# Kernel tuning notes

Measured on AMD Instinct MI355X. Metric: run time of the kernel, lower is better.

Reference implementation:

```python
import jax, jax.numpy as jnp
import numpy as np

GRID_DIM = 32      # output crop size
RES = 0.25         # A per voxel
CUBES = 5          # cubes_around_atoms_dim
NUM_CH = 5
BOX = 20.0         # dumb coords pin extents to [-20, 20]^3
LATO = 2 * CUBES + 1                      # 11
D = int(2 * BOX / RES) + 2 * (CUBES + 1) + 1  # 173, static full grid dim


def setup_inputs() -> dict:
    key = jax.random.key(0)
    k1, k2 = jax.random.split(key)
    B, N = 8, 64
    coords = jax.random.uniform(k1, (B, N, 3), jnp.float32, -7.5, 7.5)
    atoms_channel = jax.random.randint(k2, (B, N), 0, NUM_CH).astype(jnp.int32)
    radius = jnp.full((B, N), 0.5, jnp.float32)
    return {"coords": coords, "atoms_channel": atoms_channel, "radius": radius}


def _add_dumb_coords(coords, atoms_channel, radius):
    B = coords.shape[0]
    coords = jnp.concatenate(
        [coords, jnp.full((B, 1, 3), -BOX, coords.dtype), jnp.full((B, 1, 3), BOX, coords.dtype)], axis=1)
    atoms_channel = jnp.concatenate([atoms_channel, jnp.zeros((B, 2), atoms_channel.dtype)], axis=1)
    radius = jnp.concatenate([radius, jnp.full((B, 2), 0.5, radius.dtype)], axis=1)
    return coords, atoms_channel, radius


def reference(coords, atoms_channel, radius):
    coords, atoms_channel, radius = _add_dumb_coords(coords, atoms_channel, radius)
    B, M, _ = coords.shape
    # coordinates in voxel units; translation puts min corner at CUBES+1 cells
    scaled = (coords + BOX) / RES + (CUBES + 1)            # [B,M,3]
    base = jnp.floor(scaled).astype(jnp.int32)             # host voxel of each atom
    r = np.arange(-CUBES, CUBES + 1)
    off = jnp.asarray(np.stack(np.meshgrid(r, r, r, indexing='ij'), -1).reshape(-1, 3), jnp.int32)  # [K,3]
    cell = base[:, :, None, :] + off[None, None]           # [B,M,K,3] grid cells touched
    # squared distance (in A^2) from atom to cell centers; avoids sqrt (smooth at 0)
    delta = scaled[:, :, None, :] - (cell.astype(jnp.float32) + 0.5)
    d2 = jnp.sum(delta * delta, axis=-1) * (RES * RES)     # [B,M,K]
    # gaussian splat: exp(-d^2 / (2 r^2))
    val = jnp.exp(-0.5 * d2 / (radius[:, :, None] ** 2))   # [B,M,K]
    b_idx = jnp.arange(B, dtype=jnp.int32)[:, None, None]
    ch = atoms_channel[:, :, None].astype(jnp.int32)
    flat = (((b_idx * NUM_CH + ch) * D + cell[..., 0]) * D + cell[..., 1]) * D + cell[..., 2]
    vol = jnp.zeros((B * NUM_CH * D * D * D,), jnp.float32)
    vol = vol.at[flat.reshape(-1)].add(val.reshape(-1), mode='drop')
    vol = vol.reshape(B, NUM_CH, D, D, D)
    c = D // 2
    lo, hi = c - GRID_DIM // 2, c + GRID_DIM // 2
    return vol[:, :, lo:hi, lo:hi, lo:hi]
```

## Files before the change

kernel.cpp:

```cpp
#include <hip/hip_runtime.h>

#define B_DIM      8
#define N_ATOMS    64
#define NUM_CH     5
#define GRID_DIM   32
#define CROP_LO    70
#define CROP_HI    101
#define CUBES      5
#define LATO       11
#define KCELLS     (LATO*LATO*LATO)

__global__ __launch_bounds__(256) void zero_out_kernel(float4* __restrict__ out, int n4) {
    int i = blockIdx.x * blockDim.x + threadIdx.x;
    if (i < n4) out[i] = make_float4(0.f, 0.f, 0.f, 0.f);
}

__global__ __launch_bounds__(256) void splat_kernel(
    const float* __restrict__ coords,
    const int*   __restrict__ channel,
    const float* __restrict__ radius,
    float* __restrict__ out)
{
    const int atom = blockIdx.x;
    const int b    = atom >> 6;

    const float sx = coords[3*atom + 0] * 4.0f + 86.0f;
    const float sy = coords[3*atom + 1] * 4.0f + 86.0f;
    const float sz = coords[3*atom + 2] * 4.0f + 86.0f;
    const int bx = (int)floorf(sx);
    const int by = (int)floorf(sy);
    const int bz = (int)floorf(sz);

    if (bx + CUBES < CROP_LO || bx - CUBES > CROP_HI ||
        by + CUBES < CROP_LO || by - CUBES > CROP_HI ||
        bz + CUBES < CROP_LO || bz - CUBES > CROP_HI) return;

    const float r  = radius[atom];
    const float karg = -0.5f * 0.0625f / (r * r);
    const int ch = channel[atom];
    float* outBase = out + ((size_t)(b * NUM_CH + ch)) * (GRID_DIM*GRID_DIM*GRID_DIM);

    for (int k = threadIdx.x; k < KCELLS; k += 256) {
        const int i   = k / (LATO*LATO);
        const int rem = k - i * (LATO*LATO);
        const int j   = rem / LATO;
        const int l   = rem - j * LATO;

        const int gx = bx - CUBES + i;
        const int gy = by - CUBES + j;
        const int gz = bz - CUBES + l;

        const unsigned ux = (unsigned)(gx - CROP_LO);
        const unsigned uy = (unsigned)(gy - CROP_LO);
        const unsigned uz = (unsigned)(gz - CROP_LO);
        if (ux < GRID_DIM && uy < GRID_DIM && uz < GRID_DIM) {
            const float dx = sx - ((float)gx + 0.5f);
            const float dy = sy - ((float)gy + 0.5f);
            const float dz = sz - ((float)gz + 0.5f);
            const float d2 = dx*dx + dy*dy + dz*dz;
            const float val = __expf(d2 * karg);
            atomicAdd(outBase + ((ux * GRID_DIM) + uy) * GRID_DIM + uz, val);
        }
    }
}

extern "C" void kernel_launch(void* const* d_in, const int* in_sizes, int n_in,
                              void* d_out, int out_size, void* d_ws, size_t ws_size,
                              hipStream_t stream) {
    const float* coords  = (const float*)d_in[0];
    const int*   channel = (const int*)d_in[1];
    const float* radius  = (const float*)d_in[2];
    float* out = (float*)d_out;

    const int n4 = out_size / 4;
    hipLaunchKernelGGL(zero_out_kernel, dim3((n4 + 255) / 256), dim3(256), 0, stream,
                       (float4*)out, n4);

    const int atoms = in_sizes[1];
    hipLaunchKernelGGL(splat_kernel, dim3(atoms), dim3(256), 0, stream,
                       coords, channel, radius, out);
}
```

Baseline: 61.09 us.

## Replace atomic scatter splat with per-voxel gather over batch atoms

Swaps the atom-centric scatter (one block per atom doing atomicAdds into a pre-zeroed output) for a voxel-centric gather: each thread owns one output voxel, loops over the 64 atoms of its batch staged in shared memory, and accumulates per-channel sums in registers. This removes the separate zero-fill kernel launch and all global atomics, and writes each output element exactly once. In exchange every voxel tests all 64 atoms, mostly just the bounds check, and the dumb-coordinate atoms are dropped on the assumption that they never reach the crop.

```diff
diff --git a/kernel.cpp b/kernel.cpp
--- a/kernel.cpp
+++ b/kernel.cpp
@@ -1,67 +1,74 @@
 #include <hip/hip_runtime.h>
 
-#define B_DIM      8
-#define N_ATOMS    64
 #define NUM_CH     5
 #define GRID_DIM   32
 #define CROP_LO    70
-#define CROP_HI    101
 #define CUBES      5
-#define LATO       11
-#define KCELLS     (LATO*LATO*LATO)
+#define VOX_PER_B  (GRID_DIM*GRID_DIM*GRID_DIM)
 
-__global__ __launch_bounds__(256) void zero_out_kernel(float4* __restrict__ out, int n4) {
-    int i = blockIdx.x * blockDim.x + threadIdx.x;
-    if (i < n4) out[i] = make_float4(0.f, 0.f, 0.f, 0.f);
-}
-
-__global__ __launch_bounds__(256) void splat_kernel(
+__global__ __launch_bounds__(256) void gather_kernel(
     const float* __restrict__ coords,
     const int*   __restrict__ channel,
     const float* __restrict__ radius,
     float* __restrict__ out)
 {
-    const int atom = blockIdx.x;
-    const int b    = atom >> 6;
+    __shared__ float s_sx[64], s_sy[64], s_sz[64], s_kg[64];
+    __shared__ int   s_bx[64], s_by[64], s_bz[64], s_ch[64];
 
-    const float sx = coords[3*atom + 0] * 4.0f + 86.0f;
-    const float sy = coords[3*atom + 1] * 4.0f + 86.0f;
-    const float sz = coords[3*atom + 2] * 4.0f + 86.0f;
-    const int bx = (int)floorf(sx);
-    const int by = (int)floorf(sy);
-    const int bz = (int)floorf(sz);
+    const int b   = blockIdx.x >> 7;
+    const int lin = ((blockIdx.x & 127) << 8) | threadIdx.x;
+    const int t   = threadIdx.x;
 
-    if (bx + CUBES < CROP_LO || bx - CUBES > CROP_HI ||
-        by + CUBES < CROP_LO || by - CUBES > CROP_HI ||
-        bz + CUBES < CROP_LO || bz - CUBES > CROP_HI) return;
+    if (t < 64) {
+        const int a = (b << 6) + t;
+        const float sx = coords[3*a + 0] * 4.0f + 86.0f;
+        const float sy = coords[3*a + 1] * 4.0f + 86.0f;
+        const float sz = coords[3*a + 2] * 4.0f + 86.0f;
+        const float r  = radius[a];
+        s_sx[t] = sx; s_sy[t] = sy; s_sz[t] = sz;
+        s_bx[t] = (int)floorf(sx);
+        s_by[t] = (int)floorf(sy);
+        s_bz[t] = (int)floorf(sz);
+        s_kg[t] = -0.03125f / (r * r);
+        s_ch[t] = channel[a];
+    }
+    __syncthreads();
 
-    const float r  = radius[atom];
-    const float karg = -0.5f * 0.0625f / (r * r);
-    const int ch = channel[atom];
-    float* outBase = out + ((size_t)(b * NUM_CH + ch)) * (GRID_DIM*GRID_DIM*GRID_DIM);
+    const int gx = (lin >> 10) + CROP_LO;
+    const int gy = ((lin >> 5) & 31) + CROP_LO;
+    const int gz = (lin & 31) + CROP_LO;
+    const float fx = (float)gx + 0.5f;
+    const float fy = (float)gy + 0.5f;
+    const float fz = (float)gz + 0.5f;
 
-    for (int k = threadIdx.x; k < KCELLS; k += 256) {
-        const int i   = k / (LATO*LATO);
-        const int rem = k - i * (LATO*LATO);
-        const int j   = rem / LATO;
-        const int l   = rem - j * LATO;
+    float a0 = 0.f, a1 = 0.f, a2 = 0.f, a3 = 0.f, a4 = 0.f;
 
-        const int gx = bx - CUBES + i;
-        const int gy = by - CUBES + j;
-        const int gz = bz - CUBES + l;
-
-        const unsigned ux = (unsigned)(gx - CROP_LO);
-        const unsigned uy = (unsigned)(gy - CROP_LO);
-        const unsigned uz = (unsigned)(gz - CROP_LO);
-        if (ux < GRID_DIM && uy < GRID_DIM && uz < GRID_DIM) {
-            const float dx = sx - ((float)gx + 0.5f);
-            const float dy = sy - ((float)gy + 0.5f);
-            const float dz = sz - ((float)gz + 0.5f);
-            const float d2 = dx*dx + dy*dy + dz*dz;
-            const float val = __expf(d2 * karg);
-            atomicAdd(outBase + ((ux * GRID_DIM) + uy) * GRID_DIM + uz, val);
+    #pragma unroll 4
+    for (int a = 0; a < 64; ++a) {
+        const bool in =
+            (unsigned)(gx - s_bx[a] + CUBES) <= 2u*CUBES &&
+            (unsigned)(gy - s_by[a] + CUBES) <= 2u*CUBES &&
+            (unsigned)(gz - s_bz[a] + CUBES) <= 2u*CUBES;
+        if (in) {
+            const float dx = s_sx[a] - fx;
+            const float dy = s_sy[a] - fy;
+            const float dz = s_sz[a] - fz;
+            const float val = __expf(s_kg[a] * (dx*dx + dy*dy + dz*dz));
+            const int ch = s_ch[a];
+            a0 += (ch == 0) ? val : 0.f;
+            a1 += (ch == 1) ? val : 0.f;
+            a2 += (ch == 2) ? val : 0.f;
+            a3 += (ch == 3) ? val : 0.f;
+            a4 += (ch == 4) ? val : 0.f;
         }
     }
+
+    float* o = out + (size_t)b * NUM_CH * VOX_PER_B + lin;
+    o[0*VOX_PER_B] = a0;
+    o[1*VOX_PER_B] = a1;
+    o[2*VOX_PER_B] = a2;
+    o[3*VOX_PER_B] = a3;
+    o[4*VOX_PER_B] = a4;
 }
 
 extern "C" void kernel_launch(void* const* d_in, const int* in_sizes, int n_in,
@@ -72,11 +79,7 @@
     const float* radius  = (const float*)d_in[2];
     float* out = (float*)d_out;
 
-    const int n4 = out_size / 4;
-    hipLaunchKernelGGL(zero_out_kernel, dim3((n4 + 255) / 256), dim3(256), 0, stream,
-                       (float4*)out, n4);
-
-    const int atoms = in_sizes[1];
-    hipLaunchKernelGGL(splat_kernel, dim3(atoms), dim3(256), 0, stream,
+    const int B = in_sizes[1] / 64;
+    hipLaunchKernelGGL(gather_kernel, dim3(B * 128), dim3(256), 0, stream,
                        coords, channel, radius, out);
 }
```

New measurement: 64.00 us. 4.8% more time.
